# Performance work log

Measured on AMD Instinct MI355X. Metric: run time of the kernel, lower is better.

## Reference

```python
import jax, jax.numpy as jnp
import numpy as np

N_NODES = 100000
N_EDGES = 3200000
IN_DIM = 21
HID = 64


def gcn_conv(x, W, b, src, dst, n):
    # GCNConv: out = D^{-1/2} (A + I) D^{-1/2} (x W) + b
    h = x @ W  # [n, out]
    loop = jnp.arange(n)
    src_all = jnp.concatenate([src, loop])
    dst_all = jnp.concatenate([dst, loop])
    deg = jax.ops.segment_sum(jnp.ones(src_all.shape[0], h.dtype), dst_all,
                              num_segments=n)
    dinv = jax.lax.rsqrt(jnp.maximum(deg, 1.0))  # deg >= 1 with self-loops
    norm = dinv[src_all] * dinv[dst_all]  # [E+n]
    out = jax.ops.segment_sum(h[src_all] * norm[:, None], dst_all,
                              num_segments=n)
    return out + b


def setup_inputs() -> dict:
    key = jax.random.key(0)
    ks = jax.random.split(key, 12)
    def lin(k, fan_in, fan_out):
        bound = 1.0 / np.sqrt(fan_in)
        kw, kb = jax.random.split(k)
        W = jax.random.uniform(kw, (fan_in, fan_out), jnp.float32, -bound, bound)
        b = jax.random.uniform(kb, (fan_out,), jnp.float32, -bound, bound)
        return W, b
    x = jax.random.normal(ks[0], (N_NODES, IN_DIM), jnp.float32)
    edge_index = jax.random.randint(ks[1], (2, N_EDGES), 0, N_NODES, jnp.int64)
    W1, b1 = lin(ks[2], IN_DIM, HID)
    W2, b2 = lin(ks[3], HID, 2 * HID)
    W3, b3 = lin(ks[4], 2 * HID, HID)
    Wl1, bl1 = lin(ks[5], HID, 20)
    Wl2, bl2 = lin(ks[6], 20, 1)
    return {"x": x, "edge_index": edge_index,
            "W1": W1, "b1": b1, "W2": W2, "b2": b2, "W3": W3, "b3": b3,
            "Wl1": Wl1, "bl1": bl1, "Wl2": Wl2, "bl2": bl2}


def reference(x, edge_index, W1, b1, W2, b2, W3, b3, Wl1, bl1, Wl2, bl2):
    n = x.shape[0]
    src, dst = edge_index[0], edge_index[1]
    h = jax.nn.relu(gcn_conv(x, W1, b1, src, dst, n))
    h = jax.nn.relu(gcn_conv(h, W2, b2, src, dst, n))
    h = jax.nn.relu(gcn_conv(h, W3, b3, src, dst, n))
    h = jax.nn.relu(h @ Wl1 + bl1)
    return h @ Wl2 + bl2  # [n, 1]
```

## Files before the change

### kernel.cpp

```cpp
#include <hip/hip_runtime.h>

#define DEV static __device__ __forceinline__

typedef __attribute__((ext_vector_type(8))) short short8;
typedef __attribute__((ext_vector_type(4))) float f32x4;

DEV float bf2f(unsigned short u){ union{unsigned i; float f;} a; a.i=((unsigned)u)<<16; return a.f; }
DEV unsigned short f2bf(float f){ union{unsigned i; float f;} a; a.f=f; unsigned r=a.i+0x7fffu+((a.i>>16)&1u); return (unsigned short)(r>>16); }
DEV float2 bfu2f2(unsigned v){ union{unsigned i; float f;} lo,hi; lo.i=v<<16; hi.i=v&0xffff0000u; return make_float2(lo.f,hi.f); }

#define CB_SHIFT 9
#define CB_NODES 512
#define PK_SHIFT 23
#define PK_MASK  0x7fffffu
#define CHUNK 4096
#define P_WIN 4
#define BIN_CAP 18432

__global__ __launch_bounds__(256) void coarsehist_kernel(const int* __restrict__ dst,
    int* __restrict__ bcnt, int E, int NB){
  __shared__ int h[256];
  int t=threadIdx.x;
  h[t]=0; __syncthreads();
  int i=blockIdx.x*256+t, st=gridDim.x*256;
  for(;i<E;i+=st) atomicAdd(&h[dst[i]>>CB_SHIFT],1);
  __syncthreads();
  if(t<NB && h[t]) atomicAdd(&bcnt[t],h[t]);
}

__global__ __launch_bounds__(256) void binscan_kernel(const int* __restrict__ bcnt,
    int* __restrict__ binoffs, int* __restrict__ bincur, int NB, int E){
  __shared__ int s[256];
  int t=threadIdx.x;
  int v=(t<NB)?bcnt[t]:0;
  s[t]=v; __syncthreads();
  for(int o=1;o<256;o<<=1){
    int u=(t>=o)?s[t-o]:0;
    __syncthreads();
    if(t>=o) s[t]+=u;
    __syncthreads();
  }
  int ex=s[t]-v;
  if(t<NB){ binoffs[t]=ex; bincur[t]=ex; }
  if(t==0) binoffs[NB]=E;
}

__global__ __launch_bounds__(256) void chunkscatter_kernel(const int* __restrict__ src,
    const int* __restrict__ dst, int* __restrict__ bincur, unsigned* __restrict__ tmp,
    int E, int NB){
  __shared__ int lcnt[256];
  __shared__ int lstart[256];
  __shared__ int lbase[256];
  __shared__ unsigned pk[CHUNK];
  __shared__ int gaddr[CHUNK];
  int t=threadIdx.x;
  lcnt[t]=0; __syncthreads();
  int e0=blockIdx.x*CHUNK, e1=min(e0+CHUNK,E);
  int n=e1-e0;
  unsigned pkr[16]; int binr[16]; int rnk[16];
  #pragma unroll
  for(int q=0;q<16;q++){
    int i=e0+t+q*256;
    if(i<e1){
      int d=dst[i];
      int b=d>>CB_SHIFT;
      binr[q]=b;
      pkr[q]=(unsigned)src[i]|((unsigned)(d&(CB_NODES-1))<<PK_SHIFT);
      rnk[q]=atomicAdd(&lcnt[b],1);
    }
  }
  __syncthreads();
  int c=lcnt[t];
  lstart[t]=c; __syncthreads();
  for(int o=1;o<256;o<<=1){
    int u=(t>=o)?lstart[t-o]:0;
    __syncthreads();
    if(t>=o) lstart[t]+=u;
    __syncthreads();
  }
  int ex=lstart[t]-c;
  __syncthreads();
  lstart[t]=ex;
  lbase[t]=(t<NB&&c)?atomicAdd(&bincur[t],c):0;
  __syncthreads();
  #pragma unroll
  for(int q=0;q<16;q++){
    int i=e0+t+q*256;
    if(i<e1){
      int b=binr[q];
      int p=lstart[b]+rnk[q];
      pk[p]=pkr[q];
      gaddr[p]=lbase[b]+rnk[q];
    }
  }
  __syncthreads();
  for(int p=t;p<n;p+=256) tmp[gaddr[p]]=pk[p];
}

__global__ __launch_bounds__(512) void binsort_kernel(const unsigned* __restrict__ tmp,
    const int* __restrict__ binoffs, int* __restrict__ offs, int* __restrict__ deg,
    float* __restrict__ dinv, int* __restrict__ col, int M, int WSZ){
  __shared__ int cnt[CB_NODES*P_WIN];
  __shared__ int cur[CB_NODES*P_WIN];
  __shared__ int ssum[512];
  __shared__ int pkl[BIN_CAP];
  int b=blockIdx.x, t=threadIdx.x;
  int n0=b*CB_NODES;
  int e0=binoffs[b], e1=binoffs[b+1];
  int n=e1-e0;
  bool fit=(n<=BIN_CAP);
  cnt[4*t]=0; cnt[4*t+1]=0; cnt[4*t+2]=0; cnt[4*t+3]=0;
  __syncthreads();
  for(int i=e0+t;i<e1;i+=512){
    unsigned p=tmp[i];
    int s=(int)(p&PK_MASK);
    int w=(s>=WSZ)+(s>=2*WSZ)+(s>=3*WSZ);
    atomicAdd(&cnt[(int)(p>>PK_SHIFT)*P_WIN+w],1);
  }
  __syncthreads();
  int loc[4]; int s=0;
  #pragma unroll
  for(int q=0;q<4;q++){ loc[q]=s; s+=cnt[t*4+q]; }
  ssum[t]=s; __syncthreads();
  for(int o=1;o<512;o<<=1){
    int u=(t>=o)?ssum[t-o]:0;
    __syncthreads();
    if(t>=o) ssum[t]+=u;
    __syncthreads();
  }
  int rel=ssum[t]-s;
  #pragma unroll
  for(int q=0;q<4;q++) cur[t*4+q]=rel+loc[q];
  int nn=n0+t;
  if(nn<M){
    offs[nn]=e0+rel; deg[nn]=s; dinv[nn]=rsqrtf((float)(s+1));
  }
  __syncthreads();
  for(int i=e0+t;i<e1;i+=512){
    unsigned p=tmp[i];
    int s2=(int)(p&PK_MASK);
    int w=(s2>=WSZ)+(s2>=2*WSZ)+(s2>=3*WSZ);
    int pos=atomicAdd(&cur[(int)(p>>PK_SHIFT)*P_WIN+w],1);
    if(fit) pkl[pos]=s2;
    else col[e0+pos]=s2;
  }
  __syncthreads();
  if(fit){
    for(int i=t;i<n;i+=512) col[e0+i]=pkl[i];
  }
}

__global__ __launch_bounds__(256) void scale_kernel(const float* __restrict__ x, const float* __restrict__ dinv,
    uint2* __restrict__ xs, int M){
  int idx=blockIdx.x*256+threadIdx.x;
  if(idx>=M*8) return;
  int n=idx>>3, l=idx&7;
  float dv=dinv[n];
  const float* xr=x+(size_t)n*21;
  int c=4*l;
  float f0=(c  <21)?xr[c  ]*dv:0.f;
  float f1=(c+1<21)?xr[c+1]*dv:0.f;
  float f2v=(c+2<21)?xr[c+2]*dv:0.f;
  float f3=(c+3<21)?xr[c+3]*dv:0.f;
  uint2 v;
  v.x=(unsigned)f2bf(f0)|((unsigned)f2bf(f1)<<16);
  v.y=(unsigned)f2bf(f2v)|((unsigned)f2bf(f3)<<16);
  xs[(size_t)n*8+l]=v;
}

template<int GROUP,bool BR,bool OUTBF>
DEV void agg_body(const uint2* __restrict__ xs, const int* __restrict__ col,
    const int* __restrict__ offs, const int* __restrict__ deg, const float* __restrict__ dinv,
    const float* __restrict__ bias, void* __restrict__ out, int M){
  int gid=blockIdx.x*256+threadIdx.x;
  int node=gid/GROUP, lane=gid%GROUP;
  if(node>=M) return;
  float a0,a1,a2,a3;
  {
    uint2 v=xs[(size_t)node*GROUP+lane];
    float2 p=bfu2f2(v.x), q=bfu2f2(v.y);
    a0=p.x; a1=p.y; a2=q.x; a3=q.y;
  }
  int e0=offs[node], d=deg[node];
  int i=0;
  for(;i+16<=d;i+=16){
    int s[16]; uint2 w[16];
    #pragma unroll
    for(int q=0;q<16;q++) s[q]=col[e0+i+q];
    #pragma unroll
    for(int q=0;q<16;q++) w[q]=xs[(size_t)s[q]*GROUP+lane];
    #pragma unroll
    for(int q=0;q<16;q++){
      float2 p=bfu2f2(w[q].x); a0+=p.x; a1+=p.y;
      p=bfu2f2(w[q].y); a2+=p.x; a3+=p.y;
    }
  }
  for(;i+4<=d;i+=4){
    int s[4]; uint2 w[4];
    #pragma unroll
    for(int q=0;q<4;q++) s[q]=col[e0+i+q];
    #pragma unroll
    for(int q=0;q<4;q++) w[q]=xs[(size_t)s[q]*GROUP+lane];
    #pragma unroll
    for(int q=0;q<4;q++){
      float2 p=bfu2f2(w[q].x); a0+=p.x; a1+=p.y;
      p=bfu2f2(w[q].y); a2+=p.x; a3+=p.y;
    }
  }
  for(;i<d;i++){
    uint2 w=xs[(size_t)col[e0+i]*GROUP+lane];
    float2 p=bfu2f2(w.x); a0+=p.x; a1+=p.y;
    p=bfu2f2(w.y); a2+=p.x; a3+=p.y;
  }
  float dv=dinv[node];
  a0*=dv; a1*=dv; a2*=dv; a3*=dv;
  if constexpr(BR){
    a0=fmaxf(a0+bias[4*lane  ],0.f);
    a1=fmaxf(a1+bias[4*lane+1],0.f);
    a2=fmaxf(a2+bias[4*lane+2],0.f);
    a3=fmaxf(a3+bias[4*lane+3],0.f);
  }
  if constexpr(OUTBF){
    uint2 v;
    v.x=(unsigned)f2bf(a0)|((unsigned)f2bf(a1)<<16);
    v.y=(unsigned)f2bf(a2)|((unsigned)f2bf(a3)<<16);
    ((uint2*)out)[(size_t)node*GROUP+lane]=v;
  } else {
    ((float4*)out)[(size_t)node*GROUP+lane]=make_float4(a0,a1,a2,a3);
  }
}

__global__ __launch_bounds__(256) void agg1_kernel(const uint2* xs, const int* col, const int* offs,
    const int* deg, const float* dinv, uint2* out, int M){
  agg_body<8,false,true>(xs,col,offs,deg,dinv,nullptr,out,M);
}
__global__ __launch_bounds__(256) void agg2_kernel(const uint2* xs, const int* col, const int* offs,
    const int* deg, const float* dinv, uint2* out, int M){
  agg_body<16,false,true>(xs,col,offs,deg,dinv,nullptr,out,M);
}
__global__ __launch_bounds__(256) void agg3_kernel(const uint2* xs, const int* col, const int* offs,
    const int* deg, const float* dinv, const float* bias, uint2* out, int M){
  agg_body<16,true,true>(xs,col,offs,deg,dinv,bias,out,M);
}

__global__ __launch_bounds__(256) void wprep_kernel(const float* __restrict__ W,
    unsigned short* __restrict__ Warr, int KS, int RK, int N, int KN){
  int idx=blockIdx.x*256+threadIdx.x;
  if(idx>=KN) return;
  int j=idx&7, l=(idx>>3)&63, t=idx>>9;
  int ks=t%KS, nt=t/KS;
  int k=ks*32+((l>>4)<<3)+j;
  int c=nt*16+(l&15);
  float w=(k<RK)?W[(size_t)k*N+c]:0.f;
  unsigned short hi=f2bf(w);
  unsigned short lo=f2bf(w-bf2f(hi));
  Warr[idx]=hi;
  Warr[KN+idx]=lo;
}

template<int K,int NT,bool BR,bool DV>
DEV void mfma_gemm_body(const unsigned short* __restrict__ X, const unsigned short* __restrict__ Warr,
    const float* __restrict__ bias, const float* __restrict__ dinv, unsigned short* __restrict__ Out, int M){
  constexpr int KS=K/32;
  constexpr int N=NT*16;
  constexpr int KN=K*N;
  int tid=threadIdx.x;
  int lane=tid&63, wave=tid>>6;
  int rowbase=blockIdx.x*64+wave*16;
  int r=rowbase+(lane&15);
  int rc=min(r,M-1);
  const short* Xr=(const short*)(X+(size_t)rc*K+((lane>>4)<<3));
  short8 af[KS];
  #pragma unroll
  for(int ks=0;ks<KS;ks++) af[ks]=*(const short8*)(Xr+ks*32);
  const short* wp=(const short*)Warr+lane*8;
  int colv=lane&15;
  #pragma unroll
  for(int nt=0;nt<NT;nt++){
    f32x4 acc={0.f,0.f,0.f,0.f};
    const short* wnt=wp+nt*KS*512;
    #pragma unroll
    for(int ks=0;ks<KS;ks++){
      short8 bh=*(const short8*)(wnt+ks*512);
      short8 bl=*(const short8*)(wnt+KN+ks*512);
      acc=__builtin_amdgcn_mfma_f32_16x16x32_bf16(af[ks],bh,acc,0,0,0);
      acc=__builtin_amdgcn_mfma_f32_16x16x32_bf16(af[ks],bl,acc,0,0,0);
    }
    int c=nt*16+colv;
    float bv=0.f;
    if constexpr(BR) bv=bias[c];
    #pragma unroll
    for(int reg=0;reg<4;reg++){
      int row=rowbase+((lane>>4)<<2)+reg;
      if(row<M){
        float v=acc[reg];
        if constexpr(BR) v=fmaxf(v+bv,0.f);
        if constexpr(DV) v*=dinv[row];
        Out[(size_t)row*N+c]=f2bf(v);
      }
    }
  }
}

__global__ __launch_bounds__(256) void gemm1m_kernel(const unsigned short* X, const unsigned short* Warr,
    const float* bias, const float* dinv, unsigned short* Out, int M){
  mfma_gemm_body<32,4,true,true>(X,Warr,bias,dinv,Out,M);
}

__global__ __launch_bounds__(256) void gemm23_kernel(const unsigned short* __restrict__ X,
    const unsigned short* __restrict__ W2arr, const unsigned short* __restrict__ W3arr,
    const float* __restrict__ bias2, const float* __restrict__ dinv,
    unsigned short* __restrict__ Out, int M){
  __shared__ unsigned short h2t[4*16*128];
  int tid=threadIdx.x, lane=tid&63, wave=tid>>6;
  int rowbase=blockIdx.x*64+wave*16;
  unsigned short* base=h2t+wave*16*128;
  {
    int r=rowbase+(lane&15);
    int rc=min(r,M-1);
    const short* Xr=(const short*)(X+(size_t)rc*64+((lane>>4)<<3));
    short8 af0=*(const short8*)(Xr);
    short8 af1=*(const short8*)(Xr+32);
    const short* wp=(const short*)W2arr+lane*8;
    int colv=lane&15;
    #pragma unroll
    for(int nt=0;nt<8;nt++){
      f32x4 acc={0.f,0.f,0.f,0.f};
      const short* wnt=wp+nt*1024;
      short8 bh0=*(const short8*)(wnt);
      short8 bl0=*(const short8*)(wnt+8192);
      short8 bh1=*(const short8*)(wnt+512);
      short8 bl1=*(const short8*)(wnt+8704);
      acc=__builtin_amdgcn_mfma_f32_16x16x32_bf16(af0,bh0,acc,0,0,0);
      acc=__builtin_amdgcn_mfma_f32_16x16x32_bf16(af0,bl0,acc,0,0,0);
      acc=__builtin_amdgcn_mfma_f32_16x16x32_bf16(af1,bh1,acc,0,0,0);
      acc=__builtin_amdgcn_mfma_f32_16x16x32_bf16(af1,bl1,acc,0,0,0);
      int c=nt*16+colv;
      float bv=bias2[c];
      #pragma unroll
      for(int reg=0;reg<4;reg++){
        int wr=((lane>>4)<<2)+reg;
        float v=fmaxf(acc[reg]+bv,0.f);
        int e=wr*128+(((((c>>3)^(wr&7)))<<3)|(c&7));
        base[e]=f2bf(v);
      }
    }
  }
  __syncthreads();
  {
    int wr=lane&15;
    short8 af[4];
    #pragma unroll
    for(int ks=0;ks<4;ks++){
      int chunk=ks*4+(lane>>4);
      int e=wr*128+((chunk^(wr&7))<<3);
      af[ks]=*(const short8*)(base+e);
    }
    const short* wp=(const short*)W3arr+lane*8;
    int colv=lane&15;
    #pragma unroll
    for(int nt=0;nt<4;nt++){
      f32x4 acc={0.f,0.f,0.f,0.f};
      const short* wnt=wp+nt*2048;
      #pragma unroll
      for(int ks=0;ks<4;ks++){
        short8 bh=*(const short8*)(wnt+ks*512);
        short8 bl=*(const short8*)(wnt+8192+ks*512);
        acc=__builtin_amdgcn_mfma_f32_16x16x32_bf16(af[ks],bh,acc,0,0,0);
        acc=__builtin_amdgcn_mfma_f32_16x16x32_bf16(af[ks],bl,acc,0,0,0);
      }
      int c=nt*16+colv;
      #pragma unroll
      for(int reg=0;reg<4;reg++){
        int row=rowbase+((lane>>4)<<2)+reg;
        if(row<M){
          Out[(size_t)row*64+c]=f2bf(acc[reg]*dinv[row]);
        }
      }
    }
  }
}

__global__ __launch_bounds__(256) void mlp_kernel(const unsigned short* __restrict__ h, const float* __restrict__ W1,
    const float* __restrict__ b1, const float* __restrict__ W2, const float* __restrict__ b2,
    float* __restrict__ out, int M){
  __shared__ float W1s[64*20];
  __shared__ float b1s[20];
  __shared__ float W2s[20];
  __shared__ float b2s;
  int tid=threadIdx.x;
  for(int i=tid;i<1280;i+=256) W1s[i]=W1[i];
  if(tid<20){ b1s[tid]=b1[tid]; W2s[tid]=W2[tid]; }
  if(tid==0) b2s=b2[0];
  __syncthreads();
  int n=blockIdx.x*256+tid;
  if(n>=M) return;
  float acc[20];
  #pragma unroll
  for(int j=0;j<20;j++) acc[j]=b1s[j];
  const uint2* hp=(const uint2*)(h+(size_t)n*64);
  for(int k4=0;k4<16;k4++){
    uint2 v=hp[k4];
    float2 p=bfu2f2(v.x), q=bfu2f2(v.y);
    #pragma unroll
    for(int j=0;j<20;j++){
      acc[j]=fmaf(p.x,W1s[(k4*4+0)*20+j],acc[j]);
      acc[j]=fmaf(p.y,W1s[(k4*4+1)*20+j],acc[j]);
      acc[j]=fmaf(q.x,W1s[(k4*4+2)*20+j],acc[j]);
      acc[j]=fmaf(q.y,W1s[(k4*4+3)*20+j],acc[j]);
    }
  }
  float r=b2s;
  #pragma unroll
  for(int j=0;j<20;j++) r+=fmaxf(acc[j],0.f)*W2s[j];
  out[n]=r;
}

extern "C" void kernel_launch(void* const* d_in, const int* in_sizes, int n_in,
                              void* d_out, int out_size, void* d_ws, size_t ws_size,
                              hipStream_t stream){
  const float* x  =(const float*)d_in[0];
  const int*   ei =(const int*)  d_in[1];
  const float* W1 =(const float*)d_in[2];
  const float* b1 =(const float*)d_in[3];
  const float* W2 =(const float*)d_in[4];
  const float* b2 =(const float*)d_in[5];
  const float* W3 =(const float*)d_in[6];
  const float* b3 =(const float*)d_in[7];
  const float* Wl1=(const float*)d_in[8];
  const float* bl1=(const float*)d_in[9];
  const float* Wl2=(const float*)d_in[10];
  const float* bl2=(const float*)d_in[11];
  const int M=in_sizes[0]/21;
  const int E=in_sizes[1]/2;
  const int* srcp=ei;
  const int* dstp=ei+(size_t)E;
  const int NB=(M+CB_NODES-1)/CB_NODES;
  const int WSZ=(M+P_WIN-1)/P_WIN;

  char* ws=(char*)d_ws;
  size_t off=0;
  auto alloc=[&](size_t bytes)->void*{
    off=(off+255)&~(size_t)255;
    void* p=ws+off; off+=bytes; return p;
  };
  int*   offs   =(int*)  alloc((size_t)M*4);
  int*   deg    =(int*)  alloc((size_t)M*4);
  float* dinv   =(float*)alloc((size_t)M*4);
  int*   bcnt   =(int*)  alloc(256*4);
  int*   binoffs=(int*)  alloc(257*4);
  int*   bincur =(int*)  alloc(256*4);
  unsigned short* W1arr=(unsigned short*)alloc(2*32*64*2);
  unsigned short* W2arr=(unsigned short*)alloc(2*64*128*2);
  unsigned short* W3arr=(unsigned short*)alloc(2*128*64*2);
  int*   col    =(int*)  alloc((size_t)E*4);
  float* A=(float*)alloc((size_t)M*256);
  float* B=(float*)alloc((size_t)M*256);
  float* C=(float*)alloc((size_t)M*256);
  float* D=(float*)alloc((size_t)M*256);
  unsigned* tmp=(unsigned*)A;
  (void)ws_size;(void)n_in;(void)out_size;

  hipMemsetAsync(bcnt,0,256*4,stream);
  coarsehist_kernel<<<512,256,0,stream>>>(dstp,bcnt,E,NB);
  binscan_kernel<<<1,256,0,stream>>>(bcnt,binoffs,bincur,NB,E);
  chunkscatter_kernel<<<(E+CHUNK-1)/CHUNK,256,0,stream>>>(srcp,dstp,bincur,tmp,E,NB);
  binsort_kernel<<<NB,512,0,stream>>>(tmp,binoffs,offs,deg,dinv,col,M,WSZ);
  wprep_kernel<<<(32*64+255)/256,256,0,stream>>>(W1,W1arr,1,21,64,32*64);
  wprep_kernel<<<(64*128+255)/256,256,0,stream>>>(W2,W2arr,2,64,128,64*128);
  wprep_kernel<<<(128*64+255)/256,256,0,stream>>>(W3,W3arr,4,128,64,128*64);

  scale_kernel<<<(M*8+255)/256,256,0,stream>>>(x,dinv,(uint2*)A,M);
  agg1_kernel<<<(M*8+255)/256,256,0,stream>>>((const uint2*)A,col,offs,deg,dinv,(uint2*)B,M);
  gemm1m_kernel<<<(M+63)/64,256,0,stream>>>((const unsigned short*)B,W1arr,b1,dinv,(unsigned short*)C,M);
  agg2_kernel<<<(M*16+255)/256,256,0,stream>>>((const uint2*)C,col,offs,deg,dinv,(uint2*)D,M);
  gemm23_kernel<<<(M+63)/64,256,0,stream>>>((const unsigned short*)D,W2arr,W3arr,b2,dinv,(unsigned short*)B,M);
  agg3_kernel<<<(M*16+255)/256,256,0,stream>>>((const uint2*)B,col,offs,deg,dinv,b3,(uint2*)C,M);
  mlp_kernel<<<(M+255)/256,256,0,stream>>>((const unsigned short*)C,Wl1,bl1,Wl2,bl2,(float*)d_out,M);
}
```

Measured before the change: 276.9 us.

## Fuse final aggregation with MLP head using cross-lane shuffle reduction

Merges the third GCN aggregation kernel with the two-layer MLP head. Each 16-lane group computes its partial 64x20 projection and reduces it with xor shuffles, so the bf16 hidden tensor is never written and re-read and one launch disappears. The gather unroll also drops from 16 to 8 edges, lowering register pressure. In exchange the fused kernel does 20 shuffle reductions per node and stages the weights into shared memory once per block.

```diff
diff --git a/kernel.cpp b/kernel.cpp
--- a/kernel.cpp
+++ b/kernel.cpp
@@ -168,10 +168,45 @@
   xs[(size_t)n*8+l]=v;
 }
 
-template<int GROUP,bool BR,bool OUTBF>
+template<int GROUP>
+DEV void agg_gather(const uint2* __restrict__ xs, const int* __restrict__ col,
+    int e0, int d, int lane, float& a0, float& a1, float& a2, float& a3){
+  int i=0;
+  for(;i+8<=d;i+=8){
+    int s[8]; uint2 w[8];
+    #pragma unroll
+    for(int q=0;q<8;q++) s[q]=col[e0+i+q];
+    #pragma unroll
+    for(int q=0;q<8;q++) w[q]=xs[(size_t)s[q]*GROUP+lane];
+    #pragma unroll
+    for(int q=0;q<8;q++){
+      float2 p=bfu2f2(w[q].x); a0+=p.x; a1+=p.y;
+      p=bfu2f2(w[q].y); a2+=p.x; a3+=p.y;
+    }
+  }
+  for(;i+4<=d;i+=4){
+    int s[4]; uint2 w[4];
+    #pragma unroll
+    for(int q=0;q<4;q++) s[q]=col[e0+i+q];
+    #pragma unroll
+    for(int q=0;q<4;q++) w[q]=xs[(size_t)s[q]*GROUP+lane];
+    #pragma unroll
+    for(int q=0;q<4;q++){
+      float2 p=bfu2f2(w[q].x); a0+=p.x; a1+=p.y;
+      p=bfu2f2(w[q].y); a2+=p.x; a3+=p.y;
+    }
+  }
+  for(;i<d;i++){
+    uint2 w=xs[(size_t)col[e0+i]*GROUP+lane];
+    float2 p=bfu2f2(w.x); a0+=p.x; a1+=p.y;
+    p=bfu2f2(w.y); a2+=p.x; a3+=p.y;
+  }
+}
+
+template<int GROUP>
 DEV void agg_body(const uint2* __restrict__ xs, const int* __restrict__ col,
     const int* __restrict__ offs, const int* __restrict__ deg, const float* __restrict__ dinv,
-    const float* __restrict__ bias, void* __restrict__ out, int M){
+    uint2* __restrict__ out, int M){
   int gid=blockIdx.x*256+threadIdx.x;
   int node=gid/GROUP, lane=gid%GROUP;
   if(node>=M) return;
@@ -181,66 +216,72 @@
     float2 p=bfu2f2(v.x), q=bfu2f2(v.y);
     a0=p.x; a1=p.y; a2=q.x; a3=q.y;
   }
-  int e0=offs[node], d=deg[node];
-  int i=0;
-  for(;i+16<=d;i+=16){
-    int s[16]; uint2 w[16];
-    #pragma unroll
-    for(int q=0;q<16;q++) s[q]=col[e0+i+q];
-    #pragma unroll
-    for(int q=0;q<16;q++) w[q]=xs[(size_t)s[q]*GROUP+lane];
-    #pragma unroll
-    for(int q=0;q<16;q++){
-      float2 p=bfu2f2(w[q].x); a0+=p.x; a1+=p.y;
-      p=bfu2f2(w[q].y); a2+=p.x; a3+=p.y;
-    }
-  }
-  for(;i+4<=d;i+=4){
-    int s[4]; uint2 w[4];
-    #pragma unroll
-    for(int q=0;q<4;q++) s[q]=col[e0+i+q];
-    #pragma unroll
-    for(int q=0;q<4;q++) w[q]=xs[(size_t)s[q]*GROUP+lane];
-    #pragma unroll
-    for(int q=0;q<4;q++){
-      float2 p=bfu2f2(w[q].x); a0+=p.x; a1+=p.y;
-      p=bfu2f2(w[q].y); a2+=p.x; a3+=p.y;
-    }
-  }
-  for(;i<d;i++){
-    uint2 w=xs[(size_t)col[e0+i]*GROUP+lane];
-    float2 p=bfu2f2(w.x); a0+=p.x; a1+=p.y;
-    p=bfu2f2(w.y); a2+=p.x; a3+=p.y;
-  }
+  agg_gather<GROUP>(xs,col,offs[node],deg[node],lane,a0,a1,a2,a3);
   float dv=dinv[node];
   a0*=dv; a1*=dv; a2*=dv; a3*=dv;
-  if constexpr(BR){
-    a0=fmaxf(a0+bias[4*lane  ],0.f);
-    a1=fmaxf(a1+bias[4*lane+1],0.f);
-    a2=fmaxf(a2+bias[4*lane+2],0.f);
-    a3=fmaxf(a3+bias[4*lane+3],0.f);
-  }
-  if constexpr(OUTBF){
-    uint2 v;
-    v.x=(unsigned)f2bf(a0)|((unsigned)f2bf(a1)<<16);
-    v.y=(unsigned)f2bf(a2)|((unsigned)f2bf(a3)<<16);
-    ((uint2*)out)[(size_t)node*GROUP+lane]=v;
-  } else {
-    ((float4*)out)[(size_t)node*GROUP+lane]=make_float4(a0,a1,a2,a3);
-  }
+  uint2 v;
+  v.x=(unsigned)f2bf(a0)|((unsigned)f2bf(a1)<<16);
+  v.y=(unsigned)f2bf(a2)|((unsigned)f2bf(a3)<<16);
+  out[(size_t)node*GROUP+lane]=v;
 }
 
 __global__ __launch_bounds__(256) void agg1_kernel(const uint2* xs, const int* col, const int* offs,
     const int* deg, const float* dinv, uint2* out, int M){
-  agg_body<8,false,true>(xs,col,offs,deg,dinv,nullptr,out,M);
+  agg_body<8>(xs,col,offs,deg,dinv,out,M);
 }
 __global__ __launch_bounds__(256) void agg2_kernel(const uint2* xs, const int* col, const int* offs,
     const int* deg, const float* dinv, uint2* out, int M){
-  agg_body<16,false,true>(xs,col,offs,deg,dinv,nullptr,out,M);
-}
-__global__ __launch_bounds__(256) void agg3_kernel(const uint2* xs, const int* col, const int* offs,
-    const int* deg, const float* dinv, const float* bias, uint2* out, int M){
-  agg_body<16,true,true>(xs,col,offs,deg,dinv,bias,out,M);
+  agg_body<16>(xs,col,offs,deg,dinv,out,M);
+}
+
+__global__ __launch_bounds__(256) void agg3mlp_kernel(const uint2* __restrict__ xs, const int* __restrict__ col,
+    const int* __restrict__ offs, const int* __restrict__ deg, const float* __restrict__ dinv,
+    const float* __restrict__ b3, const float* __restrict__ Wl1, const float* __restrict__ bl1,
+    const float* __restrict__ Wl2, const float* __restrict__ bl2, float* __restrict__ out, int M){
+  __shared__ float W1s[64*20];
+  __shared__ float b1s[20];
+  __shared__ float W2s[20];
+  __shared__ float b2s;
+  int tid=threadIdx.x;
+  for(int i=tid;i<1280;i+=256) W1s[i]=Wl1[i];
+  if(tid<20){ b1s[tid]=bl1[tid]; W2s[tid]=Wl2[tid]; }
+  if(tid==0) b2s=bl2[0];
+  __syncthreads();
+  int gid=blockIdx.x*256+tid;
+  int node=gid/16, lane=gid%16;
+  if(node>=M) return;
+  float a0,a1,a2,a3;
+  {
+    uint2 v=xs[(size_t)node*16+lane];
+    float2 p=bfu2f2(v.x), q=bfu2f2(v.y);
+    a0=p.x; a1=p.y; a2=q.x; a3=q.y;
+  }
+  agg_gather<16>(xs,col,offs[node],deg[node],lane,a0,a1,a2,a3);
+  float dv=dinv[node];
+  a0=fmaxf(a0*dv+b3[4*lane  ],0.f);
+  a1=fmaxf(a1*dv+b3[4*lane+1],0.f);
+  a2=fmaxf(a2*dv+b3[4*lane+2],0.f);
+  a3=fmaxf(a3*dv+b3[4*lane+3],0.f);
+  float partial[20];
+  const float* w0=&W1s[(4*lane  )*20];
+  const float* w1=&W1s[(4*lane+1)*20];
+  const float* w2=&W1s[(4*lane+2)*20];
+  const float* w3=&W1s[(4*lane+3)*20];
+  #pragma unroll
+  for(int j=0;j<20;j++){
+    partial[j]=fmaf(a0,w0[j],fmaf(a1,w1[j],fmaf(a2,w2[j],a3*w3[j])));
+  }
+  #pragma unroll
+  for(int o=1;o<16;o<<=1){
+    #pragma unroll
+    for(int j=0;j<20;j++) partial[j]+=__shfl_xor(partial[j],o,16);
+  }
+  if(lane==0){
+    float r=b2s;
+    #pragma unroll
+    for(int j=0;j<20;j++) r+=fmaxf(partial[j]+b1s[j],0.f)*W2s[j];
+    out[node]=r;
+  }
 }
 
 __global__ __launch_bounds__(256) void wprep_kernel(const float* __restrict__ W,
@@ -379,41 +420,6 @@
       }
     }
   }
-}
-
-__global__ __launch_bounds__(256) void mlp_kernel(const unsigned short* __restrict__ h, const float* __restrict__ W1,
-    const float* __restrict__ b1, const float* __restrict__ W2, const float* __restrict__ b2,
-    float* __restrict__ out, int M){
-  __shared__ float W1s[64*20];
-  __shared__ float b1s[20];
-  __shared__ float W2s[20];
-  __shared__ float b2s;
-  int tid=threadIdx.x;
-  for(int i=tid;i<1280;i+=256) W1s[i]=W1[i];
-  if(tid<20){ b1s[tid]=b1[tid]; W2s[tid]=W2[tid]; }
-  if(tid==0) b2s=b2[0];
-  __syncthreads();
-  int n=blockIdx.x*256+tid;
-  if(n>=M) return;
-  float acc[20];
-  #pragma unroll
-  for(int j=0;j<20;j++) acc[j]=b1s[j];
-  const uint2* hp=(const uint2*)(h+(size_t)n*64);
-  for(int k4=0;k4<16;k4++){
-    uint2 v=hp[k4];
-    float2 p=bfu2f2(v.x), q=bfu2f2(v.y);
-    #pragma unroll
-    for(int j=0;j<20;j++){
-      acc[j]=fmaf(p.x,W1s[(k4*4+0)*20+j],acc[j]);
-      acc[j]=fmaf(p.y,W1s[(k4*4+1)*20+j],acc[j]);
-      acc[j]=fmaf(q.x,W1s[(k4*4+2)*20+j],acc[j]);
-      acc[j]=fmaf(q.y,W1s[(k4*4+3)*20+j],acc[j]);
-    }
-  }
-  float r=b2s;
-  #pragma unroll
-  for(int j=0;j<20;j++) r+=fmaxf(acc[j],0.f)*W2s[j];
-  out[n]=r;
 }
 
 extern "C" void kernel_launch(void* const* d_in, const int* in_sizes, int n_in,
@@ -475,6 +481,6 @@
   gemm1m_kernel<<<(M+63)/64,256,0,stream>>>((const unsigned short*)B,W1arr,b1,dinv,(unsigned short*)C,M);
   agg2_kernel<<<(M*16+255)/256,256,0,stream>>>((const uint2*)C,col,offs,deg,dinv,(uint2*)D,M);
   gemm23_kernel<<<(M+63)/64,256,0,stream>>>((const unsigned short*)D,W2arr,W3arr,b2,dinv,(unsigned short*)B,M);
-  agg3_kernel<<<(M*16+255)/256,256,0,stream>>>((const uint2*)B,col,offs,deg,dinv,b3,(uint2*)C,M);
-  mlp_kernel<<<(M+255)/256,256,0,stream>>>((const unsigned short*)C,Wl1,bl1,Wl2,bl2,(float*)d_out,M);
-}
+  agg3mlp_kernel<<<(M*16+255)/256,256,0,stream>>>((const uint2*)B,col,offs,deg,dinv,b3,
+      Wl1,bl1,Wl2,bl2,(float*)d_out,M);
+}
```

New measurement: 279.5 us. No clear change (+0.9%).
